# Kernel optimization log

Hardware: AMD Instinct MI355X
Metric: run time of the kernel (lower is better)

## Reference

```python
import jax, jax.numpy as jnp
import numpy as np

EPS = 1e-8


def setup_inputs() -> dict:
    key = jax.random.key(0)
    ks = jax.random.split(key, 6)
    N, H, B = 1000000, 256, 1024
    x = jax.random.normal(ks[0], (N, H), dtype=jnp.float32)
    W1 = jax.random.normal(ks[1], (H, H // 2), dtype=jnp.float32) * (1.0 / np.sqrt(H))
    b1 = jax.random.normal(ks[2], (H // 2,), dtype=jnp.float32) * 0.01
    W2 = jax.random.normal(ks[3], (H // 2, 1), dtype=jnp.float32) * (1.0 / np.sqrt(H // 2))
    b2 = jax.random.normal(ks[4], (1,), dtype=jnp.float32) * 0.01
    batch = jnp.sort(jax.random.randint(ks[5], (N,), 0, B, dtype=jnp.int64))
    return {"x": x, "W1": W1, "b1": b1, "W2": W2, "b2": b2,
            "batch": batch, "batch_size": B}


def reference(x, W1, b1, W2, b2, batch, batch_size):
    # attention MLP: Linear -> Tanh -> Linear -> softmax over all nodes (dim 0)
    scores = jnp.tanh(x @ W1 + b1) @ W2 + b2          # [N, 1]
    w = jax.nn.softmax(scores, axis=0)[:, 0]           # [N]
    # per-graph normalization (segment sums replace the dense one-hot mask)
    seg_sum = jax.ops.segment_sum(w, batch, num_segments=batch_size)  # [B]
    w_norm = w / (seg_sum[batch] + EPS)                # [N]
    # weighted per-graph feature aggregation
    graph_embedding = jax.ops.segment_sum(w_norm[:, None] * x, batch,
                                          num_segments=batch_size)   # [B, H]
    return graph_embedding
```

## Files before the change

### kernel.cpp

```cpp
#include <hip/hip_runtime.h>
#include <hip/hip_bf16.h>
#include <cstdint>


#define H_DIM 256
#define HID   128
#define CHUNK 64

typedef _Float16 half8 __attribute__((ext_vector_type(8)));
typedef float floatx4 __attribute__((ext_vector_type(4)));

__device__ __forceinline__ float fast_tanh(float y) {
    float e2 = __expf(2.0f * y);
    return 1.0f - 2.0f / (e2 + 1.0f);
}

__global__ void prep_w1(const float* __restrict__ W1, _Float16* __restrict__ w1h) {
    int idx = blockIdx.x * blockDim.x + threadIdx.x;
    if (idx >= 8 * 8 * 64 * 8) return;
    int j  = idx & 7;
    int l  = (idx >> 3) & 63;
    int ks = (idx >> 9) & 7;
    int nt = idx >> 12;
    int k = ks * 32 + ((l >> 4) << 3) + j;
    int n = nt * 16 + (l & 15);
    w1h[idx] = (_Float16)W1[k * HID + n];
}

__global__ __launch_bounds__(256, 2) void fused_kernel(
    const float* __restrict__ x, const _Float16* __restrict__ w1h,
    const float* __restrict__ b1, const float* __restrict__ W2,
    const float* __restrict__ b2, const int* __restrict__ batch,
    float* __restrict__ out, int N)
{
    __shared__ __align__(16) _Float16 w1s[32768];
    __shared__ float sbuf[CHUNK];
    __shared__ float wbuf[CHUNK];
    __shared__ float fstate;
    __shared__ float zstate;

    int tid = threadIdx.x;
    int b = blockIdx.x;

    {
        const uint4* src = (const uint4*)w1h;
        uint4* dst = (uint4*)w1s;
#pragma unroll
        for (int i = 0; i < 16; ++i) dst[tid + i * 256] = src[tid + i * 256];
    }

    int lo = 0, hi = N;
    while (lo < hi) { int mid = (lo + hi) >> 1; if (batch[mid] < b) lo = mid + 1; else hi = mid; }
    int start = lo; hi = N;
    while (lo < hi) { int mid = (lo + hi) >> 1; if (batch[mid] <= b) lo = mid + 1; else hi = mid; }
    int end = lo;
    int seglen = end - start;

    if (seglen <= 0) { out[(size_t)b * H_DIM + tid] = 0.0f; return; }

    __syncthreads();

    int wave = tid >> 6, lane = tid & 63;
    int g = lane >> 4, c = lane & 15;

    float b1r[8], w2r[8];
#pragma unroll
    for (int nt = 0; nt < 8; ++nt) { b1r[nt] = b1[nt * 16 + c]; w2r[nt] = W2[nt * 16 + c]; }
    float b2v = b2[0];

    float m_run = -3.0e38f;
    float Zrun  = 0.0f;
    float accv  = 0.0f;

    for (int co = 0; co < seglen; co += CHUNK) {
        int cnt = min(CHUNK, seglen - co);

        int row = start + co + wave * 16 + c;
        if (row > end - 1) row = end - 1;
        const float* xr = x + (size_t)row * H_DIM;

        floatx4 acc[8];
#pragma unroll
        for (int nt = 0; nt < 8; ++nt)
#pragma unroll
            for (int q = 0; q < 4; ++q) acc[nt][q] = 0.0f;

#pragma unroll
        for (int ks = 0; ks < 8; ++ks) {
            int kb = ks * 32 + g * 8;
            float4 a0 = *(const float4*)(xr + kb);
            float4 a1 = *(const float4*)(xr + kb + 4);
            half8 af;
            af[0] = (_Float16)a0.x; af[1] = (_Float16)a0.y;
            af[2] = (_Float16)a0.z; af[3] = (_Float16)a0.w;
            af[4] = (_Float16)a1.x; af[5] = (_Float16)a1.y;
            af[6] = (_Float16)a1.z; af[7] = (_Float16)a1.w;
#pragma unroll
            for (int nt = 0; nt < 8; ++nt) {
                half8 bf = *(const half8*)&w1s[((nt * 8 + ks) * 64 + lane) * 8];
                acc[nt] = __builtin_amdgcn_mfma_f32_16x16x32_f16(af, bf, acc[nt], 0, 0, 0);
            }
        }

#pragma unroll
        for (int r = 0; r < 4; ++r) {
            float p = 0.0f;
#pragma unroll
            for (int nt = 0; nt < 8; ++nt)
                p += fast_tanh(acc[nt][r] + b1r[nt]) * w2r[nt];
            p += __shfl_xor(p, 8);
            p += __shfl_xor(p, 4);
            p += __shfl_xor(p, 2);
            p += __shfl_xor(p, 1);
            if (c == 0) {
                int nl = wave * 16 + g * 4 + r;
                sbuf[nl] = (nl < cnt) ? (p + b2v) : -3.0e38f;
            }
        }
        __syncthreads();

        if (wave == 0) {
            float sv = sbuf[lane];
            float cm = sv;
#pragma unroll
            for (int off = 32; off; off >>= 1) cm = fmaxf(cm, __shfl_xor(cm, off));
            float m_new = fmaxf(m_run, cm);
            float f = __expf(m_run - m_new);
            float w = __expf(sv - m_new);
            wbuf[lane] = w;
            float sw = w;
#pragma unroll
            for (int off = 32; off; off >>= 1) sw += __shfl_xor(sw, off);
            Zrun = Zrun * f + sw;
            m_run = m_new;
            if (lane == 0) fstate = f;
        }
        __syncthreads();

        float f = fstate;
        const float* xc = x + (size_t)(start + co) * H_DIM + tid;
        float a = 0.0f;
#pragma unroll 8
        for (int j = 0; j < cnt; ++j)
            a = fmaf(wbuf[j], xc[(size_t)j * H_DIM], a);
        accv = accv * f + a;
    }

    if (tid == 0) zstate = Zrun;
    __syncthreads();
    out[(size_t)b * H_DIM + tid] = accv / zstate;
}

extern "C" void kernel_launch(void* const* d_in, const int* in_sizes, int n_in,
                              void* d_out, int out_size, void* d_ws, size_t ws_size,
                              hipStream_t stream) {
    const float* x    = (const float*)d_in[0];
    const float* W1   = (const float*)d_in[1];
    const float* b1   = (const float*)d_in[2];
    const float* W2   = (const float*)d_in[3];
    const float* b2   = (const float*)d_in[4];
    const int*   batch = (const int*)d_in[5];
    int N = in_sizes[5];
    int B = out_size / H_DIM;

    _Float16* w1h = (_Float16*)d_ws;

    prep_w1<<<32768 / 256, 256, 0, stream>>>(W1, w1h);
    fused_kernel<<<B, 256, 0, stream>>>(x, w1h, b1, W2, b2, batch, (float*)d_out, N);
}
```

Baseline: 373.8 us.

## Stage x chunks in LDS as fp16 and keep W1 slices in registers

Measured after the change: 396.7 us. 6.1% more time.

```diff
diff --git a/kernel.cpp b/kernel.cpp
--- a/kernel.cpp
+++ b/kernel.cpp
@@ -6,8 +6,10 @@
 #define H_DIM 256
 #define HID   128
 #define CHUNK 64
+#define XT_STRIDE 264
 
 typedef _Float16 half8 __attribute__((ext_vector_type(8)));
+typedef _Float16 half4 __attribute__((ext_vector_type(4)));
 typedef float floatx4 __attribute__((ext_vector_type(4)));
 
 __device__ __forceinline__ float fast_tanh(float y) {
@@ -27,27 +29,19 @@
     w1h[idx] = (_Float16)W1[k * HID + n];
 }
 
-__global__ __launch_bounds__(256, 2) void fused_kernel(
+__global__ __launch_bounds__(256, 4) void fused_kernel(
     const float* __restrict__ x, const _Float16* __restrict__ w1h,
     const float* __restrict__ b1, const float* __restrict__ W2,
     const float* __restrict__ b2, const int* __restrict__ batch,
     float* __restrict__ out, int N)
 {
-    __shared__ __align__(16) _Float16 w1s[32768];
-    __shared__ float sbuf[CHUNK];
+    __shared__ __align__(16) _Float16 xt[CHUNK * XT_STRIDE];
+    __shared__ float pbuf[4][CHUNK];
     __shared__ float wbuf[CHUNK];
-    __shared__ float fstate;
-    __shared__ float zstate;
+    __shared__ float fz[2];
 
-    int tid = threadIdx.x;
-    int b = blockIdx.x;
-
-    {
-        const uint4* src = (const uint4*)w1h;
-        uint4* dst = (uint4*)w1s;
-#pragma unroll
-        for (int i = 0; i < 16; ++i) dst[tid + i * 256] = src[tid + i * 256];
-    }
+    int tid = threadIdx.x, b = blockIdx.x;
+    int wave = tid >> 6, lane = tid & 63, g = lane >> 4, c = lane & 15;
 
     int lo = 0, hi = N;
     while (lo < hi) { int mid = (lo + hi) >> 1; if (batch[mid] < b) lo = mid + 1; else hi = mid; }
@@ -55,17 +49,21 @@
     while (lo < hi) { int mid = (lo + hi) >> 1; if (batch[mid] <= b) lo = mid + 1; else hi = mid; }
     int end = lo;
     int seglen = end - start;
-
     if (seglen <= 0) { out[(size_t)b * H_DIM + tid] = 0.0f; return; }
 
-    __syncthreads();
+    half8 bfr[2][8];
+#pragma unroll
+    for (int nt2 = 0; nt2 < 2; ++nt2)
+#pragma unroll
+        for (int ks = 0; ks < 8; ++ks)
+            bfr[nt2][ks] = *(const half8*)&w1h[(((2 * wave + nt2) * 8 + ks) * 64 + lane) * 8];
 
-    int wave = tid >> 6, lane = tid & 63;
-    int g = lane >> 4, c = lane & 15;
-
-    float b1r[8], w2r[8];
+    float b1r[2], w2r[2];
 #pragma unroll
-    for (int nt = 0; nt < 8; ++nt) { b1r[nt] = b1[nt * 16 + c]; w2r[nt] = W2[nt * 16 + c]; }
+    for (int nt2 = 0; nt2 < 2; ++nt2) {
+        b1r[nt2] = b1[(2 * wave + nt2) * 16 + c];
+        w2r[nt2] = W2[(2 * wave + nt2) * 16 + c];
+    }
     float b2v = b2[0];
 
     float m_run = -3.0e38f;
@@ -75,52 +73,69 @@
     for (int co = 0; co < seglen; co += CHUNK) {
         int cnt = min(CHUNK, seglen - co);
 
-        int row = start + co + wave * 16 + c;
-        if (row > end - 1) row = end - 1;
-        const float* xr = x + (size_t)row * H_DIM;
+        __syncthreads();
 
-        floatx4 acc[8];
 #pragma unroll
-        for (int nt = 0; nt < 8; ++nt)
+        for (int hb = 0; hb < 2; ++hb) {
+            float4 rv[8];
 #pragma unroll
-            for (int q = 0; q < 4; ++q) acc[nt][q] = 0.0f;
+            for (int i = 0; i < 8; ++i) {
+                int fi = tid + (hb * 8 + i) * 256;
+                int row = fi >> 6, col4 = fi & 63;
+                int rr = row < cnt ? row : cnt - 1;
+                rv[i] = *(const float4*)(x + (size_t)(start + co + rr) * H_DIM + col4 * 4);
+            }
+#pragma unroll
+            for (int i = 0; i < 8; ++i) {
+                int fi = tid + (hb * 8 + i) * 256;
+                int row = fi >> 6, col4 = fi & 63;
+                half4 hv;
+                hv[0] = (_Float16)rv[i].x; hv[1] = (_Float16)rv[i].y;
+                hv[2] = (_Float16)rv[i].z; hv[3] = (_Float16)rv[i].w;
+                *(half4*)&xt[row * XT_STRIDE + col4 * 4] = hv;
+            }
+        }
+
+        __syncthreads();
+
+        floatx4 acc[4][2];
+#pragma unroll
+        for (int mt = 0; mt < 4; ++mt)
+#pragma unroll
+            for (int nt2 = 0; nt2 < 2; ++nt2)
+#pragma unroll
+                for (int q = 0; q < 4; ++q) acc[mt][nt2][q] = 0.0f;
 
 #pragma unroll
         for (int ks = 0; ks < 8; ++ks) {
-            int kb = ks * 32 + g * 8;
-            float4 a0 = *(const float4*)(xr + kb);
-            float4 a1 = *(const float4*)(xr + kb + 4);
-            half8 af;
-            af[0] = (_Float16)a0.x; af[1] = (_Float16)a0.y;
-            af[2] = (_Float16)a0.z; af[3] = (_Float16)a0.w;
-            af[4] = (_Float16)a1.x; af[5] = (_Float16)a1.y;
-            af[6] = (_Float16)a1.z; af[7] = (_Float16)a1.w;
 #pragma unroll
-            for (int nt = 0; nt < 8; ++nt) {
-                half8 bf = *(const half8*)&w1s[((nt * 8 + ks) * 64 + lane) * 8];
-                acc[nt] = __builtin_amdgcn_mfma_f32_16x16x32_f16(af, bf, acc[nt], 0, 0, 0);
+            for (int mt = 0; mt < 4; ++mt) {
+                half8 af = *(const half8*)&xt[(mt * 16 + c) * XT_STRIDE + ks * 32 + g * 8];
+                acc[mt][0] = __builtin_amdgcn_mfma_f32_16x16x32_f16(af, bfr[0][ks], acc[mt][0], 0, 0, 0);
+                acc[mt][1] = __builtin_amdgcn_mfma_f32_16x16x32_f16(af, bfr[1][ks], acc[mt][1], 0, 0, 0);
             }
         }
 
 #pragma unroll
-        for (int r = 0; r < 4; ++r) {
-            float p = 0.0f;
+        for (int mt = 0; mt < 4; ++mt) {
 #pragma unroll
-            for (int nt = 0; nt < 8; ++nt)
-                p += fast_tanh(acc[nt][r] + b1r[nt]) * w2r[nt];
-            p += __shfl_xor(p, 8);
-            p += __shfl_xor(p, 4);
-            p += __shfl_xor(p, 2);
-            p += __shfl_xor(p, 1);
-            if (c == 0) {
-                int nl = wave * 16 + g * 4 + r;
-                sbuf[nl] = (nl < cnt) ? (p + b2v) : -3.0e38f;
+            for (int r = 0; r < 4; ++r) {
+                float p = fast_tanh(acc[mt][0][r] + b1r[0]) * w2r[0]
+                        + fast_tanh(acc[mt][1][r] + b1r[1]) * w2r[1];
+                p += __shfl_xor(p, 8);
+                p += __shfl_xor(p, 4);
+                p += __shfl_xor(p, 2);
+                p += __shfl_xor(p, 1);
+                if (c == 0) pbuf[wave][mt * 16 + g * 4 + r] = p;
             }
         }
+
         __syncthreads();
 
         if (wave == 0) {
-            float sv = sbuf[lane];
+            float sv = (lane < cnt)
+                ? (pbuf[0][lane] + pbuf[1][lane] + pbuf[2][lane] + pbuf[3][lane] + b2v)
+                : -3.0e38f;
             float cm = sv;
 #pragma unroll
             for (int off = 32; off; off >>= 1) cm = fmaxf(cm, __shfl_xor(cm, off));
@@ -133,22 +148,22 @@
             for (int off = 32; off; off >>= 1) sw += __shfl_xor(sw, off);
             Zrun = Zrun * f + sw;
             m_run = m_new;
-            if (lane == 0) fstate = f;
+            if (lane == 0) fz[0] = f;
         }
+
         __syncthreads();
 
-        float f = fstate;
-        const float* xc = x + (size_t)(start + co) * H_DIM + tid;
+        float f = fz[0];
         float a = 0.0f;
 #pragma unroll 8
-        for (int j = 0; j < cnt; ++j)
-            a = fmaf(wbuf[j], xc[(size_t)j * H_DIM], a);
+        for (int j = 0; j < CHUNK; ++j)
+            a = fmaf(wbuf[j], (float)xt[j * XT_STRIDE + tid], a);
         accv = accv * f + a;
     }
 
-    if (tid == 0) zstate = Zrun;
+    if (tid == 0) fz[1] = Zrun;
     __syncthreads();
-    out[(size_t)b * H_DIM + tid] = accv / zstate;
+    out[(size_t)b * H_DIM + tid] = accv / fz[1];
 }
 
 extern "C" void kernel_launch(void* const* d_in, const int* in_sizes, int n_in,
```

## Fuse score and aggregation into one pass reusing fp16 x fragments

Applied to the files above, without the earlier changes.

New measurement: 934.0 us. 150% more time.

```diff
diff --git a/kernel.cpp b/kernel.cpp
--- a/kernel.cpp
+++ b/kernel.cpp
@@ -1,11 +1,9 @@
 #include <hip/hip_runtime.h>
-#include <hip/hip_bf16.h>
 #include <cstdint>
 
 
 #define H_DIM 256
 #define HID   128
-#define CHUNK 64
 
 typedef _Float16 half8 __attribute__((ext_vector_type(8)));
 typedef float floatx4 __attribute__((ext_vector_type(4)));
@@ -27,128 +25,169 @@
     w1h[idx] = (_Float16)W1[k * HID + n];
 }
 
-__global__ __launch_bounds__(256, 2) void fused_kernel(
+__global__ __launch_bounds__(512, 2) void fused_kernel(
     const float* __restrict__ x, const _Float16* __restrict__ w1h,
     const float* __restrict__ b1, const float* __restrict__ W2,
     const float* __restrict__ b2, const int* __restrict__ batch,
-    float* __restrict__ out, int N)
+    float* __restrict__ out, int N, int B)
 {
     __shared__ __align__(16) _Float16 w1s[32768];
-    __shared__ float sbuf[CHUNK];
-    __shared__ float wbuf[CHUNK];
-    __shared__ float fstate;
-    __shared__ float zstate;
+    __shared__ float scr[8 * H_DIM + 8];
 
     int tid = threadIdx.x;
-    int b = blockIdx.x;
-
     {
-        const uint4* src = (const uint4*)w1h;
-        uint4* dst = (uint4*)w1s;
-#pragma unroll
-        for (int i = 0; i < 16; ++i) dst[tid + i * 256] = src[tid + i * 256];
+        const uint4* s = (const uint4*)w1h;
+        uint4* d = (uint4*)w1s;
+#pragma unroll
+        for (int i = 0; i < 8; ++i) d[tid + i * 512] = s[tid + i * 512];
     }
-
-    int lo = 0, hi = N;
-    while (lo < hi) { int mid = (lo + hi) >> 1; if (batch[mid] < b) lo = mid + 1; else hi = mid; }
-    int start = lo; hi = N;
-    while (lo < hi) { int mid = (lo + hi) >> 1; if (batch[mid] <= b) lo = mid + 1; else hi = mid; }
-    int end = lo;
-    int seglen = end - start;
-
-    if (seglen <= 0) { out[(size_t)b * H_DIM + tid] = 0.0f; return; }
-
     __syncthreads();
 
-    int wave = tid >> 6, lane = tid & 63;
-    int g = lane >> 4, c = lane & 15;
+    int wv = tid >> 6, lane = tid & 63, g = lane >> 4, c = lane & 15;
 
     float b1r[8], w2r[8];
 #pragma unroll
-    for (int nt = 0; nt < 8; ++nt) { b1r[nt] = b1[nt * 16 + c]; w2r[nt] = W2[nt * 16 + c]; }
+    for (int nt = 0; nt < 8; ++nt) {
+        b1r[nt] = b1[nt * 16 + c];
+        w2r[nt] = W2[nt * 16 + c];
+    }
     float b2v = b2[0];
 
-    float m_run = -3.0e38f;
-    float Zrun  = 0.0f;
-    float accv  = 0.0f;
-
-    for (int co = 0; co < seglen; co += CHUNK) {
-        int cnt = min(CHUNK, seglen - co);
-
-        int row = start + co + wave * 16 + c;
-        if (row > end - 1) row = end - 1;
-        const float* xr = x + (size_t)row * H_DIM;
-
-        floatx4 acc[8];
-#pragma unroll
-        for (int nt = 0; nt < 8; ++nt)
-#pragma unroll
-            for (int q = 0; q < 4; ++q) acc[nt][q] = 0.0f;
-
-#pragma unroll
-        for (int ks = 0; ks < 8; ++ks) {
-            int kb = ks * 32 + g * 8;
-            float4 a0 = *(const float4*)(xr + kb);
-            float4 a1 = *(const float4*)(xr + kb + 4);
-            half8 af;
-            af[0] = (_Float16)a0.x; af[1] = (_Float16)a0.y;
-            af[2] = (_Float16)a0.z; af[3] = (_Float16)a0.w;
-            af[4] = (_Float16)a1.x; af[5] = (_Float16)a1.y;
-            af[6] = (_Float16)a1.z; af[7] = (_Float16)a1.w;
+    for (int gi = 0; gi < 4; ++gi) {
+        int b = blockIdx.x * 4 + gi;
+        if (b >= B) break;
+
+        int lo = 0, hi = N;
+        while (lo < hi) { int m = (lo + hi) >> 1; if (batch[m] < b) lo = m + 1; else hi = m; }
+        int start = lo; hi = N;
+        while (lo < hi) { int m = (lo + hi) >> 1; if (batch[m] <= b) lo = m + 1; else hi = m; }
+        int end = lo;
+        int seglen = end - start;
+
+        if (seglen <= 0) {
+            if (tid < H_DIM) out[(size_t)b * H_DIM + tid] = 0.0f;
+            __syncthreads();
+            continue;
+        }
+        int ntiles = (seglen + 31) >> 5;
+
+        float accv[8][8];
+#pragma unroll
+        for (int ks = 0; ks < 8; ++ks)
+#pragma unroll
+            for (int j = 0; j < 8; ++j) accv[ks][j] = 0.0f;
+        float zp = 0.0f;
+
+        for (int t = wv; t < ntiles; t += 8) {
+            int r0 = start + t * 32;
+            int ra = r0 + c, rb = r0 + 16 + c;
+            int rl = end - 1;
+            int ca = ra <= rl ? ra : rl;
+            int cb = rb <= rl ? rb : rl;
+            const float* pa = x + (size_t)ca * H_DIM + g * 8;
+            const float* pb = x + (size_t)cb * H_DIM + g * 8;
+
+            float4 qa[16];
+#pragma unroll
+            for (int ks = 0; ks < 8; ++ks) {
+                qa[2 * ks]     = *(const float4*)(pa + ks * 32);
+                qa[2 * ks + 1] = *(const float4*)(pa + ks * 32 + 4);
+            }
+            half8 af0[8];
+#pragma unroll
+            for (int ks = 0; ks < 8; ++ks) {
+                half8 h;
+                h[0] = (_Float16)qa[2 * ks].x;     h[1] = (_Float16)qa[2 * ks].y;
+                h[2] = (_Float16)qa[2 * ks].z;     h[3] = (_Float16)qa[2 * ks].w;
+                h[4] = (_Float16)qa[2 * ks + 1].x; h[5] = (_Float16)qa[2 * ks + 1].y;
+                h[6] = (_Float16)qa[2 * ks + 1].z; h[7] = (_Float16)qa[2 * ks + 1].w;
+                af0[ks] = h;
+            }
+#pragma unroll
+            for (int ks = 0; ks < 8; ++ks) {
+                qa[2 * ks]     = *(const float4*)(pb + ks * 32);
+                qa[2 * ks + 1] = *(const float4*)(pb + ks * 32 + 4);
+            }
+            half8 af1[8];
+#pragma unroll
+            for (int ks = 0; ks < 8; ++ks) {
+                half8 h;
+                h[0] = (_Float16)qa[2 * ks].x;     h[1] = (_Float16)qa[2 * ks].y;
+                h[2] = (_Float16)qa[2 * ks].z;     h[3] = (_Float16)qa[2 * ks].w;
+                h[4] = (_Float16)qa[2 * ks + 1].x; h[5] = (_Float16)qa[2 * ks + 1].y;
+                h[6] = (_Float16)qa[2 * ks + 1].z; h[7] = (_Float16)qa[2 * ks + 1].w;
+                af1[ks] = h;
+            }
+
+            float p0[4] = {0, 0, 0, 0}, p1[4] = {0, 0, 0, 0};
 #pragma unroll
             for (int nt = 0; nt < 8; ++nt) {
-                half8 bf = *(const half8*)&w1s[((nt * 8 + ks) * 64 + lane) * 8];
-                acc[nt] = __builtin_amdgcn_mfma_f32_16x16x32_f16(af, bf, acc[nt], 0, 0, 0);
-            }
+                floatx4 s0 = {0, 0, 0, 0}, s1 = {0, 0, 0, 0};
+#pragma unroll
+                for (int ks = 0; ks < 8; ++ks) {
+                    half8 bf = *(const half8*)&w1s[((nt * 8 + ks) * 64 + lane) * 8];
+                    s0 = __builtin_amdgcn_mfma_f32_16x16x32_f16(af0[ks], bf, s0, 0, 0, 0);
+                    s1 = __builtin_amdgcn_mfma_f32_16x16x32_f16(af1[ks], bf, s1, 0, 0, 0);
+                }
+#pragma unroll
+                for (int r = 0; r < 4; ++r) {
+                    p0[r] += fast_tanh(s0[r] + b1r[nt]) * w2r[nt];
+                    p1[r] += fast_tanh(s1[r] + b1r[nt]) * w2r[nt];
+                }
+            }
+#pragma unroll
+            for (int r = 0; r < 4; ++r) {
+                p0[r] += __shfl_xor(p0[r], 1); p0[r] += __shfl_xor(p0[r], 2);
+                p0[r] += __shfl_xor(p0[r], 4); p0[r] += __shfl_xor(p0[r], 8);
+                p1[r] += __shfl_xor(p1[r], 1); p1[r] += __shfl_xor(p1[r], 2);
+                p1[r] += __shfl_xor(p1[r], 4); p1[r] += __shfl_xor(p1[r], 8);
+            }
+            float sel0 = (lane & 1) ? p0[1] : p0[0];
+            float t0b  = (lane & 1) ? p0[3] : p0[2];
+            sel0 = (lane & 2) ? t0b : sel0;
+            float sel1 = (lane & 1) ? p1[1] : p1[0];
+            float t1b  = (lane & 1) ? p1[3] : p1[2];
+            sel1 = (lane & 2) ? t1b : sel1;
+            int src = ((lane & 15) >> 2) * 16 + (lane & 3);
+            float s_a = __shfl(sel0, src) + b2v;
+            float s_b = __shfl(sel1, src) + b2v;
+            float w0 = (ra < end) ? __expf(s_a) : 0.0f;
+            float w1 = (rb < end) ? __expf(s_b) : 0.0f;
+            if (g == 0) zp += w0 + w1;
+
+#pragma unroll
+            for (int ks = 0; ks < 8; ++ks)
+#pragma unroll
+                for (int j = 0; j < 8; ++j)
+                    accv[ks][j] += w0 * (float)af0[ks][j] + w1 * (float)af1[ks][j];
         }
 
 #pragma unroll
-        for (int r = 0; r < 4; ++r) {
-            float p = 0.0f;
-#pragma unroll
-            for (int nt = 0; nt < 8; ++nt)
-                p += fast_tanh(acc[nt][r] + b1r[nt]) * w2r[nt];
-            p += __shfl_xor(p, 8);
-            p += __shfl_xor(p, 4);
-            p += __shfl_xor(p, 2);
-            p += __shfl_xor(p, 1);
-            if (c == 0) {
-                int nl = wave * 16 + g * 4 + r;
-                sbuf[nl] = (nl < cnt) ? (p + b2v) : -3.0e38f;
-            }
+        for (int ks = 0; ks < 8; ++ks)
+#pragma unroll
+            for (int j = 0; j < 8; ++j) {
+                float v = accv[ks][j];
+                v += __shfl_xor(v, 1); v += __shfl_xor(v, 2);
+                v += __shfl_xor(v, 4); v += __shfl_xor(v, 8);
+                if (c == ((ks * 8 + j) & 15))
+                    scr[wv * H_DIM + ks * 32 + g * 8 + j] = v;
+            }
+        float z = zp;
+        z += __shfl_xor(z, 1);  z += __shfl_xor(z, 2);  z += __shfl_xor(z, 4);
+        z += __shfl_xor(z, 8);  z += __shfl_xor(z, 16); z += __shfl_xor(z, 32);
+        if (lane == 0) scr[8 * H_DIM + wv] = z;
+        __syncthreads();
+        if (tid < H_DIM) {
+            float s = 0.0f;
+#pragma unroll
+            for (int w = 0; w < 8; ++w) s += scr[w * H_DIM + tid];
+            float Z = 0.0f;
+#pragma unroll
+            for (int w = 0; w < 8; ++w) Z += scr[8 * H_DIM + w];
+            out[(size_t)b * H_DIM + tid] = s / Z;
         }
         __syncthreads();
-
-        if (wave == 0) {
-            float sv = sbuf[lane];
-            float cm = sv;
-#pragma unroll
-            for (int off = 32; off; off >>= 1) cm = fmaxf(cm, __shfl_xor(cm, off));
-            float m_new = fmaxf(m_run, cm);
-            float f = __expf(m_run - m_new);
-            float w = __expf(sv - m_new);
-            wbuf[lane] = w;
-            float sw = w;
-#pragma unroll
-            for (int off = 32; off; off >>= 1) sw += __shfl_xor(sw, off);
-            Zrun = Zrun * f + sw;
-            m_run = m_new;
-            if (lane == 0) fstate = f;
-        }
-        __syncthreads();
-
-        float f = fstate;
-        const float* xc = x + (size_t)(start + co) * H_DIM + tid;
-        float a = 0.0f;
-#pragma unroll 8
-        for (int j = 0; j < cnt; ++j)
-            a = fmaf(wbuf[j], xc[(size_t)j * H_DIM], a);
-        accv = accv * f + a;
     }
-
-    if (tid == 0) zstate = Zrun;
-    __syncthreads();
-    out[(size_t)b * H_DIM + tid] = accv / zstate;
 }
 
 extern "C" void kernel_launch(void* const* d_in, const int* in_sizes, int n_in,
@@ -166,5 +205,7 @@
     _Float16* w1h = (_Float16*)d_ws;
 
     prep_w1<<<32768 / 256, 256, 0, stream>>>(W1, w1h);
-    fused_kernel<<<B, 256, 0, stream>>>(x, w1h, b1, W2, b2, batch, (float*)d_out, N);
-}
+    int nblk = (B + 3) / 4;
+    fused_kernel<<<nblk, 512, 0, stream>>>(x, w1h, b1, W2, b2, batch,
+                                           (float*)d_out, N, B);
+}
```

## Stage x tiles once in LDS as fp16 and keep W1 in registers

Applied to the files above, without the earlier changes.

After: 540.5 us. 1.45x slower.

```diff
diff --git a/kernel.cpp b/kernel.cpp
--- a/kernel.cpp
+++ b/kernel.cpp
@@ -1,11 +1,10 @@
 #include <hip/hip_runtime.h>
-#include <hip/hip_bf16.h>
 #include <cstdint>
 
 
 #define H_DIM 256
 #define HID   128
-#define CHUNK 64
+#define ROWS  64
 
 typedef _Float16 half8 __attribute__((ext_vector_type(8)));
 typedef float floatx4 __attribute__((ext_vector_type(4)));
@@ -13,6 +12,11 @@
 __device__ __forceinline__ float fast_tanh(float y) {
     float e2 = __expf(2.0f * y);
     return 1.0f - 2.0f / (e2 + 1.0f);
+}
+
+__device__ __forceinline__ void light_barrier() {
+    asm volatile("s_waitcnt lgkmcnt(0)" ::: "memory");
+    __builtin_amdgcn_s_barrier();
 }
 
 __global__ void prep_w1(const float* __restrict__ W1, _Float16* __restrict__ w1h) {
@@ -27,128 +31,127 @@
     w1h[idx] = (_Float16)W1[k * HID + n];
 }
 
-__global__ __launch_bounds__(256, 2) void fused_kernel(
+__global__ __launch_bounds__(512, 2) void fused_kernel(
     const float* __restrict__ x, const _Float16* __restrict__ w1h,
     const float* __restrict__ b1, const float* __restrict__ W2,
     const float* __restrict__ b2, const int* __restrict__ batch,
     float* __restrict__ out, int N)
 {
-    __shared__ __align__(16) _Float16 w1s[32768];
-    __shared__ float sbuf[CHUNK];
-    __shared__ float wbuf[CHUNK];
-    __shared__ float fstate;
-    __shared__ float zstate;
+    __shared__ __align__(16) _Float16 xt[2][ROWS * H_DIM];
+    __shared__ float pbuf[8][ROWS];
+    __shared__ float wbuf[ROWS];
 
-    int tid = threadIdx.x;
-    int b = blockIdx.x;
+    int tid = threadIdx.x, b = blockIdx.x;
+    int wv = tid >> 6, lane = tid & 63, g = lane >> 4, c = lane & 15;
 
-    {
-        const uint4* src = (const uint4*)w1h;
-        uint4* dst = (uint4*)w1s;
+    int lo = 0, hi = N;
+    while (lo < hi) { int m = (lo + hi) >> 1; if (batch[m] < b) lo = m + 1; else hi = m; }
+    int start = lo; hi = N;
+    while (lo < hi) { int m = (lo + hi) >> 1; if (batch[m] <= b) lo = m + 1; else hi = m; }
+    int end = lo;
+    int seglen = end - start;
+    if (seglen <= 0) {
+        if (tid < H_DIM) out[(size_t)b * H_DIM + tid] = 0.0f;
+        return;
+    }
+    int nch = (seglen + ROWS - 1) / ROWS;
+
+    half8 bfr[8];
 #pragma unroll
-        for (int i = 0; i < 16; ++i) dst[tid + i * 256] = src[tid + i * 256];
+    for (int ks = 0; ks < 8; ++ks)
+        bfr[ks] = *(const half8*)&w1h[((wv * 8 + ks) * 64 + lane) * 8];
+    float b1v = b1[wv * 16 + c];
+    float w2v = W2[wv * 16 + c];
+    float b2v = b2[0];
+
+    int srow = tid >> 3, q = tid & 7;
+    int pcol = tid & 255, prh = tid >> 8;
+
+    float acc = 0.0f;
+    float zp  = 0.0f;
+
+    auto load = [&](float4* r, int t) {
+        int cntt = seglen - t * ROWS; if (cntt > ROWS) cntt = ROWS;
+        int lr = srow < cntt ? srow : cntt - 1;
+        const float* p = x + (size_t)(start + t * ROWS + lr) * H_DIM + q * 32;
+#pragma unroll
+        for (int i = 0; i < 8; ++i) r[i] = *(const float4*)(p + i * 4);
+    };
+    auto stage = [&](const float4* r, _Float16* xb) {
+#pragma unroll
+        for (int i8 = 0; i8 < 4; ++i8) {
+            half8 hv;
+            hv[0] = (_Float16)r[2 * i8].x;     hv[1] = (_Float16)r[2 * i8].y;
+            hv[2] = (_Float16)r[2 * i8].z;     hv[3] = (_Float16)r[2 * i8].w;
+            hv[4] = (_Float16)r[2 * i8 + 1].x; hv[5] = (_Float16)r[2 * i8 + 1].y;
+            hv[6] = (_Float16)r[2 * i8 + 1].z; hv[7] = (_Float16)r[2 * i8 + 1].w;
+            int byt = srow * 512 + ((q * 64 + i8 * 16) ^ ((srow & 7) << 6));
+            *(half8*)((char*)xb + byt) = hv;
+        }
+    };
+
+    float4 cA[8], cB[8];
+    load(cA, 0);
+
+    for (int t = 0; t < nch; ++t) {
+        _Float16* xb = xt[t & 1];
+        int cnt = seglen - t * ROWS; if (cnt > ROWS) cnt = ROWS;
+
+        if (t & 1) { if (t + 1 < nch) load(cA, t + 1); stage(cB, xb); }
+        else       { if (t + 1 < nch) load(cB, t + 1); stage(cA, xb); }
+        light_barrier();
+
+#pragma unroll
+        for (int mt = 0; mt < 4; ++mt) {
+            int row = mt * 16 + c;
+            const char* base = (const char*)xb + row * 512;
+            floatx4 sacc = {0.0f, 0.0f, 0.0f, 0.0f};
+#pragma unroll
+            for (int ks = 0; ks < 8; ++ks) {
+                int byt = (ks * 64 + g * 16) ^ ((row & 7) << 6);
+                half8 af = *(const half8*)(base + byt);
+                sacc = __builtin_amdgcn_mfma_f32_16x16x32_f16(af, bfr[ks], sacc, 0, 0, 0);
+            }
+#pragma unroll
+            for (int r = 0; r < 4; ++r) {
+                float p = fast_tanh(sacc[r] + b1v) * w2v;
+                p += __shfl_xor(p, 1); p += __shfl_xor(p, 2);
+                p += __shfl_xor(p, 4); p += __shfl_xor(p, 8);
+                if (c == 0) pbuf[wv][mt * 16 + g * 4 + r] = p;
+            }
+        }
+        light_barrier();
+
+        if (tid < ROWS) {
+            float s = b2v;
+#pragma unroll
+            for (int w = 0; w < 8; ++w) s += pbuf[w][tid];
+            float e = (tid < cnt) ? __expf(s) : 0.0f;
+            wbuf[tid] = e;
+            zp += e;
+        }
+        light_barrier();
+
+#pragma unroll
+        for (int j = 0; j < 32; ++j) {
+            int row = prh * 32 + j;
+            int byt = row * 512 + ((pcol * 2) ^ ((row & 7) << 6));
+            acc = fmaf(wbuf[row], (float)*(const _Float16*)((const char*)xb + byt), acc);
+        }
     }
 
-    int lo = 0, hi = N;
-    while (lo < hi) { int mid = (lo + hi) >> 1; if (batch[mid] < b) lo = mid + 1; else hi = mid; }
-    int start = lo; hi = N;
-    while (lo < hi) { int mid = (lo + hi) >> 1; if (batch[mid] <= b) lo = mid + 1; else hi = mid; }
-    int end = lo;
-    int seglen = end - start;
-
-    if (seglen <= 0) { out[(size_t)b * H_DIM + tid] = 0.0f; return; }
-
     __syncthreads();
-
-    int wave = tid >> 6, lane = tid & 63;
-    int g = lane >> 4, c = lane & 15;
-
-    float b1r[8], w2r[8];
-#pragma unroll
-    for (int nt = 0; nt < 8; ++nt) { b1r[nt] = b1[nt * 16 + c]; w2r[nt] = W2[nt * 16 + c]; }
-    float b2v = b2[0];
-
-    float m_run = -3.0e38f;
-    float Zrun  = 0.0f;
-    float accv  = 0.0f;
-
-    for (int co = 0; co < seglen; co += CHUNK) {
-        int cnt = min(CHUNK, seglen - co);
-
-        int row = start + co + wave * 16 + c;
-        if (row > end - 1) row = end - 1;
-        const float* xr = x + (size_t)row * H_DIM;
-
-        floatx4 acc[8];
-#pragma unroll
-        for (int nt = 0; nt < 8; ++nt)
-#pragma unroll
-            for (int q = 0; q < 4; ++q) acc[nt][q] = 0.0f;
-
-#pragma unroll
-        for (int ks = 0; ks < 8; ++ks) {
-            int kb = ks * 32 + g * 8;
-            float4 a0 = *(const float4*)(xr + kb);
-            float4 a1 = *(const float4*)(xr + kb + 4);
-            half8 af;
-            af[0] = (_Float16)a0.x; af[1] = (_Float16)a0.y;
-            af[2] = (_Float16)a0.z; af[3] = (_Float16)a0.w;
-            af[4] = (_Float16)a1.x; af[5] = (_Float16)a1.y;
-            af[6] = (_Float16)a1.z; af[7] = (_Float16)a1.w;
-#pragma unroll
-            for (int nt = 0; nt < 8; ++nt) {
-                half8 bf = *(const half8*)&w1s[((nt * 8 + ks) * 64 + lane) * 8];
-                acc[nt] = __builtin_amdgcn_mfma_f32_16x16x32_f16(af, bf, acc[nt], 0, 0, 0);
-            }
-        }
-
-#pragma unroll
-        for (int r = 0; r < 4; ++r) {
-            float p = 0.0f;
-#pragma unroll
-            for (int nt = 0; nt < 8; ++nt)
-                p += fast_tanh(acc[nt][r] + b1r[nt]) * w2r[nt];
-            p += __shfl_xor(p, 8);
-            p += __shfl_xor(p, 4);
-            p += __shfl_xor(p, 2);
-            p += __shfl_xor(p, 1);
-            if (c == 0) {
-                int nl = wave * 16 + g * 4 + r;
-                sbuf[nl] = (nl < cnt) ? (p + b2v) : -3.0e38f;
-            }
-        }
-        __syncthreads();
-
-        if (wave == 0) {
-            float sv = sbuf[lane];
-            float cm = sv;
-#pragma unroll
-            for (int off = 32; off; off >>= 1) cm = fmaxf(cm, __shfl_xor(cm, off));
-            float m_new = fmaxf(m_run, cm);
-            float f = __expf(m_run - m_new);
-            float w = __expf(sv - m_new);
-            wbuf[lane] = w;
-            float sw = w;
-#pragma unroll
-            for (int off = 32; off; off >>= 1) sw += __shfl_xor(sw, off);
-            Zrun = Zrun * f + sw;
-            m_run = m_new;
-            if (lane == 0) fstate = f;
-        }
-        __syncthreads();
-
-        float f = fstate;
-        const float* xc = x + (size_t)(start + co) * H_DIM + tid;
-        float a = 0.0f;
-#pragma unroll 8
-        for (int j = 0; j < cnt; ++j)
-            a = fmaf(wbuf[j], xc[(size_t)j * H_DIM], a);
-        accv = accv * f + a;
+    float* scr = &pbuf[0][0];
+    scr[tid] = acc;
+    if (wv == 0) {
+        float z = zp;
+        z += __shfl_xor(z, 1);  z += __shfl_xor(z, 2);  z += __shfl_xor(z, 4);
+        z += __shfl_xor(z, 8);  z += __shfl_xor(z, 16); z += __shfl_xor(z, 32);
+        if (lane == 0) wbuf[0] = z;
     }
-
-    if (tid == 0) zstate = Zrun;
     __syncthreads();
-    out[(size_t)b * H_DIM + tid] = accv / zstate;
+    if (tid < H_DIM)
+        out[(size_t)b * H_DIM + tid] = (scr[tid] + scr[tid + 256]) / wbuf[0];
 }
 
 extern "C" void kernel_launch(void* const* d_in, const int* in_sizes, int n_in,
@@ -166,5 +169,6 @@
     _Float16* w1h = (_Float16*)d_ws;
 
     prep_w1<<<32768 / 256, 256, 0, stream>>>(W1, w1h);
-    fused_kernel<<<B, 256, 0, stream>>>(x, w1h, b1, W2, b2, batch, (float*)d_out, N);
+    fused_kernel<<<B, 512, 0, stream>>>(x, w1h, b1, W2, b2, batch,
+                                        (float*)d_out, N);
 }
```
